# Performance work log

Hardware: AMD Instinct MI355X
Metric: run time of the kernel (lower is better)

The kernel has to match this reference:

```python
import jax, jax.numpy as jnp
import numpy as np


def _pool2(x):
    # 2x2 max pool, stride 2 (matches F.max_pool2d(x, 2))
    b, c, h, w = x.shape
    return x.reshape(b, c, h // 2, 2, w // 2, 2).max(axis=(3, 5))


def setup_inputs() -> dict:
    key = jax.random.key(0)
    ks = jax.random.split(key, 6)
    B, C, H, W = 16, 512, 64, 64
    x = jax.random.normal(ks[0], (B, C, H, W), dtype=jnp.float32)
    scale = 0.02
    theta_w = jax.random.normal(ks[1], (C // 8, C), dtype=jnp.float32) * scale
    phi_w = jax.random.normal(ks[2], (C // 8, C), dtype=jnp.float32) * scale
    g_w = jax.random.normal(ks[3], (C // 2, C), dtype=jnp.float32) * scale
    o_w = jax.random.normal(ks[4], (C, C // 2), dtype=jnp.float32) * scale
    # original inits gamma=0; use a nonzero value so output depends on attention path
    gamma = jax.random.normal(ks[5], (), dtype=jnp.float32) * 0.5
    return {"x": x, "theta_w": theta_w, "phi_w": phi_w, "g_w": g_w, "o_w": o_w, "gamma": gamma}


def reference(x, theta_w, phi_w, g_w, o_w, gamma):
    B, C, H, W = x.shape
    HW = H * W
    # 1x1 convs == channel GEMMs
    theta = jnp.einsum('bchw,kc->bkhw', x, theta_w).reshape(B, C // 8, HW).transpose(0, 2, 1)  # [B, HW, C/8]
    phi = _pool2(jnp.einsum('bchw,kc->bkhw', x, phi_w)).reshape(B, C // 8, HW // 4)            # [B, C/8, HW/4]
    beta = jax.nn.softmax(jnp.einsum('bnk,bkm->bnm', theta, phi), axis=-1)                     # [B, HW, HW/4]
    g = _pool2(jnp.einsum('bchw,kc->bkhw', x, g_w)).reshape(B, C // 2, HW // 4)                # [B, C/2, HW/4]
    # g.bmm(beta^T): contract over pooled positions m -> [B, C/2, HW]
    o_in = jnp.einsum('bcm,bnm->bcn', g, beta).reshape(B, C // 2, H, W)
    o = jnp.einsum('bchw,kc->bkhw', o_in, o_w)                                                 # [B, C, H, W]
    return gamma * o + x
```

## Files before the change

### kernel.cpp

```cpp
#include <hip/hip_runtime.h>

#define B_   16
#define C_   512
#define HW_  4096
#define M_   1024
#define TPAD 136

typedef __attribute__((ext_vector_type(8))) short bf16x8;
typedef __attribute__((ext_vector_type(4))) float f32x4;

static __device__ __forceinline__ unsigned short f2bf(float f) {
    union { float f; unsigned u; } v; v.f = f;
    unsigned r = v.u + 0x7fffu + ((v.u >> 16) & 1u);
    return (unsigned short)(r >> 16);
}
static __device__ __forceinline__ float bf2f(unsigned short h) {
    union { unsigned u; float f; } v; v.u = ((unsigned)h) << 16;
    return v.f;
}
static __device__ __forceinline__ void gload_lds16(const void* g, void* l) {
    __builtin_amdgcn_global_load_lds(
        (const __attribute__((address_space(1))) unsigned int*)g,
        (__attribute__((address_space(3))) unsigned int*)l, 16, 0, 0);
}

__global__ __launch_bounds__(256) void k_weights(
    const float* __restrict__ thw, const float* __restrict__ phw,
    const float* __restrict__ gw,  const float* __restrict__ ow,
    unsigned short* __restrict__ Wb, unsigned short* __restrict__ oWb,
    unsigned short* __restrict__ g_p) {
    int i = blockIdx.x * 256 + threadIdx.x;
    if (i < 32768)        Wb[i] = f2bf(thw[i]);
    else if (i < 65536)   Wb[i] = f2bf(phw[i - 32768]);
    else if (i < 196608)  Wb[i] = f2bf(gw[i - 65536]);
    else if (i < 327680)  oWb[i - 196608] = f2bf(ow[i - 196608]);
    else if (i < 589824) {
        int i2 = i - 327680;
        int b = i2 >> 14;
        int r = (i2 >> 10) & 15;
        int m = i2 & 1023;
        g_p[((size_t)b * 272 + 256 + r) * M_ + m] =
            (r == 0) ? (unsigned short)0x3F80u : (unsigned short)0;
    }
}

__global__ __launch_bounds__(256) void k_transpose_x(
    const float* __restrict__ x, unsigned short* __restrict__ xT) {
    __shared__ float tile[64][65];
    int b = blockIdx.z, c0 = blockIdx.y * 64, hw0 = blockIdx.x * 64;
    const float* xb = x + ((size_t)b * C_ + c0) * HW_ + hw0;
    int t = threadIdx.x;
    int r = t >> 4, c4 = (t & 15) * 4;
#pragma unroll
    for (int k = 0; k < 4; k++) {
        int row = r + k * 16;
        float4 v = *reinterpret_cast<const float4*>(xb + (size_t)row * HW_ + c4);
        tile[row][c4 + 0] = v.x; tile[row][c4 + 1] = v.y;
        tile[row][c4 + 2] = v.z; tile[row][c4 + 3] = v.w;
    }
    __syncthreads();
    unsigned short* o = xT + ((size_t)b * HW_ + hw0) * C_ + c0;
#pragma unroll
    for (int k = 0; k < 4; k++) {
        int hwr = r + k * 16;
        ushort4 u;
        u.x = f2bf(tile[c4 + 0][hwr]); u.y = f2bf(tile[c4 + 1][hwr]);
        u.z = f2bf(tile[c4 + 2][hwr]); u.w = f2bf(tile[c4 + 3][hwr]);
        *reinterpret_cast<ushort4*>(o + (size_t)hwr * C_ + c4) = u;
    }
}

__global__ __launch_bounds__(256, 4) void k_proj(
    const unsigned short* __restrict__ xT, const unsigned short* __restrict__ Wb,
    unsigned short* __restrict__ theta_n, unsigned short* __restrict__ phi_p,
    unsigned short* __restrict__ g_p) {
    __shared__ unsigned short smem[128 * TPAD];
    unsigned short* As = smem;
    unsigned short* Bs = smem + 8192;

    int b = blockIdx.z, mt = blockIdx.y, bx = blockIdx.x;
    int hw0 = bx * 128;
    int tid = threadIdx.x, w = tid >> 6, lane = tid & 63;
    int l15 = lane & 15, q = lane >> 4;
    int wr = w >> 1, wc = w & 1;

    const unsigned short* Ab = Wb + (size_t)(mt * 128) * 512;
    const unsigned short* Bb = xT + ((size_t)b * HW_ + hw0) * 512;
    int trow = tid >> 3, tch = tid & 7;

    f32x4 acc[4][4] = {};
    for (int ks = 0; ks < 8; ks++) {
        int k0 = ks * 64;
        if (ks) __syncthreads();
#pragma unroll
        for (int i = 0; i < 4; i++) {
            int row = i * 32 + trow;
            int ch = tch ^ (row & 7);
            gload_lds16(Ab + (size_t)row * 512 + k0 + ch * 8, &As[(i * 256 + w * 64) * 8]);
        }
#pragma unroll
        for (int i = 0; i < 4; i++) {
            int row = i * 32 + trow;
            int ch = tch ^ (row & 7);
            gload_lds16(Bb + (size_t)row * 512 + k0 + ch * 8, &Bs[(i * 256 + w * 64) * 8]);
        }
        __syncthreads();
#pragma unroll
        for (int kk = 0; kk < 2; kk++) {
            bf16x8 af[4], bfr[4];
#pragma unroll
            for (int mi = 0; mi < 4; mi++) {
                int row = wr * 64 + mi * 16 + l15;
                int ch = (kk * 4 + q) ^ (row & 7);
                af[mi] = *(const bf16x8*)&As[row * 64 + ch * 8];
            }
#pragma unroll
            for (int ni = 0; ni < 4; ni++) {
                int row = wc * 64 + ni * 16 + l15;
                int ch = (kk * 4 + q) ^ (row & 7);
                bfr[ni] = *(const bf16x8*)&Bs[row * 64 + ch * 8];
            }
#pragma unroll
            for (int mi = 0; mi < 4; mi++)
#pragma unroll
                for (int ni = 0; ni < 4; ni++)
                    acc[mi][ni] = __builtin_amdgcn_mfma_f32_16x16x32_bf16(
                        af[mi], bfr[ni], acc[mi][ni], 0, 0, 0);
        }
    }

    __syncthreads();
#pragma unroll
    for (int mi = 0; mi < 4; mi++)
#pragma unroll
        for (int ni = 0; ni < 4; ni++) {
            int col = wc * 64 + ni * 16 + l15;
            int row = wr * 64 + mi * 16 + q * 4;
            ushort4 u;
            u.x = f2bf(acc[mi][ni][0]); u.y = f2bf(acc[mi][ni][1]);
            u.z = f2bf(acc[mi][ni][2]); u.w = f2bf(acc[mi][ni][3]);
            *reinterpret_cast<ushort4*>(&smem[col * TPAD + row]) = u;
        }
    __syncthreads();

    if (mt == 0) {
        int hw_l = tid >> 1, kh = (tid & 1) * 32;
        const unsigned short* srcp = &smem[hw_l * TPAD + kh];
        unsigned short* dstp = theta_n + ((size_t)b * HW_ + hw0 + hw_l) * 64 + kh;
#pragma unroll
        for (int i = 0; i < 4; i++)
            *reinterpret_cast<uint4*>(dstp + i * 8) =
                *reinterpret_cast<const uint4*>(srcp + i * 8);
        int pc = tid & 63, mg = tid >> 6;
#pragma unroll
        for (int j = 0; j < 8; j++) {
            int m_l = mg * 8 + j, w_ = m_l * 2;
            float v0 = bf2f(smem[(w_)      * TPAD + 64 + pc]);
            float v1 = bf2f(smem[(w_ + 1)  * TPAD + 64 + pc]);
            float v2 = bf2f(smem[(64 + w_) * TPAD + 64 + pc]);
            float v3 = bf2f(smem[(65 + w_) * TPAD + 64 + pc]);
            float v = fmaxf(fmaxf(v0, v1), fmaxf(v2, v3));
            phi_p[((size_t)b * M_ + bx * 32 + m_l) * 64 + pc] = f2bf(v);
        }
    } else {
        int lr = tid & 127, half = tid >> 7;
        int gc = (mt - 1) * 128 + lr;
        unsigned short* dst = g_p + ((size_t)b * 272 + gc) * M_ + bx * 32 + half * 16;
        unsigned short tmp[16];
#pragma unroll
        for (int i = 0; i < 16; i++) {
            int w_ = (half * 16 + i) * 2;
            float v0 = bf2f(smem[(w_)      * TPAD + lr]);
            float v1 = bf2f(smem[(w_ + 1)  * TPAD + lr]);
            float v2 = bf2f(smem[(64 + w_) * TPAD + lr]);
            float v3 = bf2f(smem[(65 + w_) * TPAD + lr]);
            tmp[i] = f2bf(fmaxf(fmaxf(v0, v1), fmaxf(v2, v3)));
        }
#pragma unroll
        for (int i = 0; i < 4; i++)
            *reinterpret_cast<ushort4*>(dst + i * 4) =
                *reinterpret_cast<const ushort4*>(&tmp[i * 4]);
    }
}

__global__ __launch_bounds__(512, 4) void k_attn(
    const unsigned short* __restrict__ theta_n, const unsigned short* __restrict__ phi_p,
    const unsigned short* __restrict__ g_p, unsigned short* __restrict__ o_in) {
    __shared__ unsigned short phi_s[64 * 64];
    __shared__ unsigned short g_s[272 * 64];
    __shared__ unsigned short p_lds[8][16][88];

    int b = blockIdx.y, n0 = blockIdx.x * 128;
    int tid = threadIdx.x, w = tid >> 6, lane = tid & 63;
    int l15 = lane & 15, q = lane >> 4;
    int nw = n0 + w * 16;

    const unsigned short* th = theta_n + ((size_t)b * HW_ + nw + l15) * 64 + q * 8;
    bf16x8 a0 = *(const bf16x8*)(th);
    bf16x8 a1 = *(const bf16x8*)(th + 32);

    const unsigned short* phib = phi_p + (size_t)b * M_ * 64;
    const unsigned short* gb   = g_p   + (size_t)b * 272 * M_;

    int sw = l15 & 7;

    f32x4 acc[17] = {};
    for (int mc = 0; mc < 16; mc++) {
        int m0 = mc * 64;
        __syncthreads();
        {
            int p = tid;
            int row = p >> 3, ch = (p & 7) ^ (row & 7);
            gload_lds16(phib + (size_t)(m0 + row) * 64 + ch * 8, &phi_s[w * 512]);
        }
#pragma unroll
        for (int it = 0; it < 5; it++) {
            int s = w + it * 8;
            if (s < 34) {
                int row = s * 8 + (lane >> 3);
                int ch = (lane & 7) ^ (row & 7);
                gload_lds16(gb + (size_t)row * M_ + m0 + ch * 8, &g_s[s * 512]);
            }
        }
        __syncthreads();

#pragma unroll
        for (int f = 0; f < 4; f++) {
            const unsigned short* pr = &phi_s[(f * 16 + l15) * 64];
            bf16x8 b0 = *(const bf16x8*)(pr + (q ^ sw) * 8);
            bf16x8 b1 = *(const bf16x8*)(pr + ((q + 4) ^ sw) * 8);
            f32x4 s = {};
            s = __builtin_amdgcn_mfma_f32_16x16x32_bf16(a0, b0, s, 0, 0, 0);
            s = __builtin_amdgcn_mfma_f32_16x16x32_bf16(a1, b1, s, 0, 0, 0);
#pragma unroll
            for (int j = 0; j < 4; j++)
                p_lds[w][q * 4 + j][f * 16 + l15] = f2bf(__expf(s[j]));
        }
        bf16x8 p0 = *(const bf16x8*)&p_lds[w][l15][q * 8];
        bf16x8 p1 = *(const bf16x8*)&p_lds[w][l15][32 + q * 8];
#pragma unroll
        for (int cf = 0; cf < 17; cf++) {
            const unsigned short* gr = &g_s[(cf * 16 + l15) * 64];
            bf16x8 g0 = *(const bf16x8*)(gr + (q ^ sw) * 8);
            bf16x8 g1 = *(const bf16x8*)(gr + ((q + 4) ^ sw) * 8);
            acc[cf] = __builtin_amdgcn_mfma_f32_16x16x32_bf16(p0, g0, acc[cf], 0, 0, 0);
            acc[cf] = __builtin_amdgcn_mfma_f32_16x16x32_bf16(p1, g1, acc[cf], 0, 0, 0);
        }
    }

    float dinv[4];
#pragma unroll
    for (int j = 0; j < 4; j++) {
        float d = __shfl(acc[16][j], (lane & 48), 64);
        dinv[j] = 1.0f / d;
    }
#pragma unroll
    for (int cf = 0; cf < 16; cf++)
#pragma unroll
        for (int j = 0; j < 4; j++)
            o_in[((size_t)b * HW_ + nw + q * 4 + j) * 256 + cf * 16 + l15] =
                f2bf(acc[cf][j] * dinv[j]);
}

__global__ __launch_bounds__(256, 4) void k_oproj(
    const unsigned short* __restrict__ o_in, const unsigned short* __restrict__ oWb,
    const float* __restrict__ x, const float* __restrict__ gamma_p,
    float* __restrict__ out) {
    __shared__ unsigned short smem[128 * TPAD];
    unsigned short* As = smem;
    unsigned short* Bs = smem + 8192;

    int b = blockIdx.z, mt = blockIdx.y, hw0 = blockIdx.x * 128;
    int tid = threadIdx.x, w = tid >> 6, lane = tid & 63;
    int l15 = lane & 15, q = lane >> 4;
    int wr = w >> 1, wc = w & 1;

    const unsigned short* Ab = oWb + (size_t)(mt * 128) * 256;
    const unsigned short* Bb = o_in + ((size_t)b * HW_ + hw0) * 256;
    int trow = tid >> 3, tch = tid & 7;

    f32x4 acc[4][4] = {};
    for (int ks = 0; ks < 4; ks++) {
        int k0 = ks * 64;
        if (ks) __syncthreads();
#pragma unroll
        for (int i = 0; i < 4; i++) {
            int row = i * 32 + trow;
            int ch = tch ^ (row & 7);
            gload_lds16(Ab + (size_t)row * 256 + k0 + ch * 8, &As[(i * 256 + w * 64) * 8]);
        }
#pragma unroll
        for (int i = 0; i < 4; i++) {
            int row = i * 32 + trow;
            int ch = tch ^ (row & 7);
            gload_lds16(Bb + (size_t)row * 256 + k0 + ch * 8, &Bs[(i * 256 + w * 64) * 8]);
        }
        __syncthreads();
#pragma unroll
        for (int kk = 0; kk < 2; kk++) {
            bf16x8 af[4], bfr[4];
#pragma unroll
            for (int mi = 0; mi < 4; mi++) {
                int row = wr * 64 + mi * 16 + l15;
                int ch = (kk * 4 + q) ^ (row & 7);
                af[mi] = *(const bf16x8*)&As[row * 64 + ch * 8];
            }
#pragma unroll
            for (int ni = 0; ni < 4; ni++) {
                int row = wc * 64 + ni * 16 + l15;
                int ch = (kk * 4 + q) ^ (row & 7);
                bfr[ni] = *(const bf16x8*)&Bs[row * 64 + ch * 8];
            }
#pragma unroll
            for (int mi = 0; mi < 4; mi++)
#pragma unroll
                for (int ni = 0; ni < 4; ni++)
                    acc[mi][ni] = __builtin_amdgcn_mfma_f32_16x16x32_bf16(
                        af[mi], bfr[ni], acc[mi][ni], 0, 0, 0);
        }
    }

    __syncthreads();
#pragma unroll
    for (int mi = 0; mi < 4; mi++)
#pragma unroll
        for (int ni = 0; ni < 4; ni++) {
            int col = wc * 64 + ni * 16 + l15;
            int rb = wr * 64 + mi * 16 + q * 4;
#pragma unroll
            for (int j = 0; j < 4; j++)
                smem[(rb + j) * TPAD + col] = f2bf(acc[mi][ni][j]);
        }
    __syncthreads();

    float gam = *gamma_p;
    int sub = tid >> 5, p32 = tid & 31;
#pragma unroll
    for (int p = 0; p < 16; p++) {
        int row = p * 8 + sub;
        ushort4 v = *reinterpret_cast<const ushort4*>(&smem[row * TPAD + p32 * 4]);
        size_t idx = ((size_t)b * C_ + mt * 128 + row) * HW_ + hw0 + p32 * 4;
        float4 xv = *reinterpret_cast<const float4*>(x + idx);
        float4 o;
        o.x = gam * bf2f(v.x) + xv.x;
        o.y = gam * bf2f(v.y) + xv.y;
        o.z = gam * bf2f(v.z) + xv.z;
        o.w = gam * bf2f(v.w) + xv.w;
        *reinterpret_cast<float4*>(out + idx) = o;
    }
}

extern "C" void kernel_launch(void* const* d_in, const int* in_sizes, int n_in,
                              void* d_out, int out_size, void* d_ws, size_t ws_size,
                              hipStream_t stream) {
    const float* x     = (const float*)d_in[0];
    const float* thw   = (const float*)d_in[1];
    const float* phw   = (const float*)d_in[2];
    const float* gw    = (const float*)d_in[3];
    const float* ow    = (const float*)d_in[4];
    const float* gamma = (const float*)d_in[5];
    float* out = (float*)d_out;

    char* ws = (char*)d_ws;
    unsigned short* xT   = (unsigned short*)(ws + 0);
    unsigned short* Wb   = (unsigned short*)(ws + 67108864);
    unsigned short* oWb  = (unsigned short*)(ws + 67502080);
    unsigned short* oin  = (unsigned short*)(ws + 67764224);
    unsigned short* thn  = (unsigned short*)(ws + 118095872);
    unsigned short* phip = (unsigned short*)(ws + 126484480);
    unsigned short* gp   = (unsigned short*)(ws + 128581632);

    hipLaunchKernelGGL(k_weights, dim3(2304), dim3(256), 0, stream, thw, phw, gw, ow, Wb, oWb, gp);
    hipLaunchKernelGGL(k_transpose_x, dim3(64, 8, 16), dim3(256), 0, stream, x, xT);
    hipLaunchKernelGGL(k_proj, dim3(32, 3, 16), dim3(256), 0, stream, xT, Wb, thn, phip, gp);
    hipLaunchKernelGGL(k_attn, dim3(32, 16), dim3(512), 0, stream, thn, phip, gp, oin);
    hipLaunchKernelGGL(k_oproj, dim3(32, 4, 16), dim3(256), 0, stream, oin, oWb, x, gamma, out);
}
```

Measured before the change: 193.6 us.

## Fuse x transpose and bf16 conversion into projection GEMM tile loads

Removes the separate transpose kernel and the bf16 xT workspace. The projection GEMM now reads fp32 x directly, converts it to bf16 and transposes it into swizzled LDS with a new bank-swizzle function. This avoids the intermediate round trip to global memory and one launch. In exchange it reads fp32 x for each of the three weight tiles and replaces async global-to-LDS loads with synchronous register loads and LDS stores.

```diff
diff --git a/kernel.cpp b/kernel.cpp
--- a/kernel.cpp
+++ b/kernel.cpp
@@ -23,6 +23,7 @@
         (const __attribute__((address_space(1))) unsigned int*)g,
         (__attribute__((address_space(3))) unsigned int*)l, 16, 0, 0);
 }
+static __device__ __forceinline__ int fb(int row) { return (row ^ (row >> 2)) & 7; }
 
 __global__ __launch_bounds__(256) void k_weights(
     const float* __restrict__ thw, const float* __restrict__ phw,
@@ -44,34 +45,8 @@
     }
 }
 
-__global__ __launch_bounds__(256) void k_transpose_x(
-    const float* __restrict__ x, unsigned short* __restrict__ xT) {
-    __shared__ float tile[64][65];
-    int b = blockIdx.z, c0 = blockIdx.y * 64, hw0 = blockIdx.x * 64;
-    const float* xb = x + ((size_t)b * C_ + c0) * HW_ + hw0;
-    int t = threadIdx.x;
-    int r = t >> 4, c4 = (t & 15) * 4;
-#pragma unroll
-    for (int k = 0; k < 4; k++) {
-        int row = r + k * 16;
-        float4 v = *reinterpret_cast<const float4*>(xb + (size_t)row * HW_ + c4);
-        tile[row][c4 + 0] = v.x; tile[row][c4 + 1] = v.y;
-        tile[row][c4 + 2] = v.z; tile[row][c4 + 3] = v.w;
-    }
-    __syncthreads();
-    unsigned short* o = xT + ((size_t)b * HW_ + hw0) * C_ + c0;
-#pragma unroll
-    for (int k = 0; k < 4; k++) {
-        int hwr = r + k * 16;
-        ushort4 u;
-        u.x = f2bf(tile[c4 + 0][hwr]); u.y = f2bf(tile[c4 + 1][hwr]);
-        u.z = f2bf(tile[c4 + 2][hwr]); u.w = f2bf(tile[c4 + 3][hwr]);
-        *reinterpret_cast<ushort4*>(o + (size_t)hwr * C_ + c4) = u;
-    }
-}
-
 __global__ __launch_bounds__(256, 4) void k_proj(
-    const unsigned short* __restrict__ xT, const unsigned short* __restrict__ Wb,
+    const float* __restrict__ x, const unsigned short* __restrict__ Wb,
     unsigned short* __restrict__ theta_n, unsigned short* __restrict__ phi_p,
     unsigned short* __restrict__ g_p) {
     __shared__ unsigned short smem[128 * TPAD];
@@ -85,8 +60,10 @@
     int wr = w >> 1, wc = w & 1;
 
     const unsigned short* Ab = Wb + (size_t)(mt * 128) * 512;
-    const unsigned short* Bb = xT + ((size_t)b * HW_ + hw0) * 512;
+    const float* xb = x + (size_t)b * C_ * HW_ + hw0;
     int trow = tid >> 3, tch = tid & 7;
+    int hg4 = (tid & 31) * 4;
+    int kq2 = (tid >> 5) * 2;
 
     f32x4 acc[4][4] = {};
     for (int ks = 0; ks < 8; ks++) {
@@ -99,10 +76,24 @@
             gload_lds16(Ab + (size_t)row * 512 + k0 + ch * 8, &As[(i * 256 + w * 64) * 8]);
         }
 #pragma unroll
-        for (int i = 0; i < 4; i++) {
-            int row = i * 32 + trow;
-            int ch = tch ^ (row & 7);
-            gload_lds16(Bb + (size_t)row * 512 + k0 + ch * 8, &Bs[(i * 256 + w * 64) * 8]);
+        for (int it = 0; it < 2; it++) {
+            int kg = kq2 + it;
+            const float* xs = xb + (size_t)(k0 + kg * 4) * HW_ + hg4;
+            float4 r0 = *reinterpret_cast<const float4*>(xs);
+            float4 r1 = *reinterpret_cast<const float4*>(xs + HW_);
+            float4 r2 = *reinterpret_cast<const float4*>(xs + 2 * HW_);
+            float4 r3 = *reinterpret_cast<const float4*>(xs + 3 * HW_);
+            const float* p0 = (const float*)&r0; const float* p1 = (const float*)&r1;
+            const float* p2 = (const float*)&r2; const float* p3 = (const float*)&r3;
+#pragma unroll
+            for (int t = 0; t < 4; t++) {
+                int row = hg4 + t;
+                int ch = (kg >> 1) ^ fb(row);
+                ushort4 u;
+                u.x = f2bf(p0[t]); u.y = f2bf(p1[t]);
+                u.z = f2bf(p2[t]); u.w = f2bf(p3[t]);
+                *reinterpret_cast<ushort4*>(&Bs[row * 64 + ch * 8 + (kg & 1) * 4]) = u;
+            }
         }
         __syncthreads();
 #pragma unroll
@@ -117,7 +108,7 @@
 #pragma unroll
             for (int ni = 0; ni < 4; ni++) {
                 int row = wc * 64 + ni * 16 + l15;
-                int ch = (kk * 4 + q) ^ (row & 7);
+                int ch = (kk * 4 + q) ^ fb(row);
                 bfr[ni] = *(const bf16x8*)&Bs[row * 64 + ch * 8];
             }
 #pragma unroll
@@ -362,17 +353,15 @@
     float* out = (float*)d_out;
 
     char* ws = (char*)d_ws;
-    unsigned short* xT   = (unsigned short*)(ws + 0);
-    unsigned short* Wb   = (unsigned short*)(ws + 67108864);
-    unsigned short* oWb  = (unsigned short*)(ws + 67502080);
-    unsigned short* oin  = (unsigned short*)(ws + 67764224);
-    unsigned short* thn  = (unsigned short*)(ws + 118095872);
-    unsigned short* phip = (unsigned short*)(ws + 126484480);
-    unsigned short* gp   = (unsigned short*)(ws + 128581632);
+    unsigned short* Wb   = (unsigned short*)(ws + 0);
+    unsigned short* oWb  = (unsigned short*)(ws + 393216);
+    unsigned short* oin  = (unsigned short*)(ws + 655360);
+    unsigned short* thn  = (unsigned short*)(ws + 34209792);
+    unsigned short* phip = (unsigned short*)(ws + 42598400);
+    unsigned short* gp   = (unsigned short*)(ws + 44695552);
 
     hipLaunchKernelGGL(k_weights, dim3(2304), dim3(256), 0, stream, thw, phw, gw, ow, Wb, oWb, gp);
-    hipLaunchKernelGGL(k_transpose_x, dim3(64, 8, 16), dim3(256), 0, stream, x, xT);
-    hipLaunchKernelGGL(k_proj, dim3(32, 3, 16), dim3(256), 0, stream, xT, Wb, thn, phip, gp);
+    hipLaunchKernelGGL(k_proj, dim3(32, 3, 16), dim3(256), 0, stream, x, Wb, thn, phip, gp);
     hipLaunchKernelGGL(k_attn, dim3(32, 16), dim3(512), 0, stream, thn, phip, gp, oin);
     hipLaunchKernelGGL(k_oproj, dim3(32, 4, 16), dim3(256), 0, stream, oin, oWb, x, gamma, out);
 }
```

Result: slower. 198.9 us (+2.7%).

## Double-buffer attention tiles and compute softmax denominator from register ones

Applied to the files above, without the earlier changes.

The attention kernel now streams phi and g in 32-wide chunks into two LDS buffers, prefetching the next chunk while computing the current one, with one barrier per iteration. The softmax row-sum, previously obtained from padded ones-rows in g_p written by the weight kernel, is now computed by an extra MFMA against an in-register ones vector. The padding-row initialization and its threads are dropped. This aims to hide global-to-LDS load latency and cut LDS traffic, at the cost of twice as many loop iterations with smaller MFMA batches. Workspace offsets are also moved.

```diff
diff --git a/kernel.cpp b/kernel.cpp
--- a/kernel.cpp
+++ b/kernel.cpp
@@ -27,21 +27,12 @@
 __global__ __launch_bounds__(256) void k_weights(
     const float* __restrict__ thw, const float* __restrict__ phw,
     const float* __restrict__ gw,  const float* __restrict__ ow,
-    unsigned short* __restrict__ Wb, unsigned short* __restrict__ oWb,
-    unsigned short* __restrict__ g_p) {
+    unsigned short* __restrict__ Wb, unsigned short* __restrict__ oWb) {
     int i = blockIdx.x * 256 + threadIdx.x;
     if (i < 32768)        Wb[i] = f2bf(thw[i]);
     else if (i < 65536)   Wb[i] = f2bf(phw[i - 32768]);
     else if (i < 196608)  Wb[i] = f2bf(gw[i - 65536]);
     else if (i < 327680)  oWb[i - 196608] = f2bf(ow[i - 196608]);
-    else if (i < 589824) {
-        int i2 = i - 327680;
-        int b = i2 >> 14;
-        int r = (i2 >> 10) & 15;
-        int m = i2 & 1023;
-        g_p[((size_t)b * 272 + 256 + r) * M_ + m] =
-            (r == 0) ? (unsigned short)0x3F80u : (unsigned short)0;
-    }
 }
 
 __global__ __launch_bounds__(256) void k_transpose_x(
@@ -186,9 +177,9 @@
 __global__ __launch_bounds__(512, 4) void k_attn(
     const unsigned short* __restrict__ theta_n, const unsigned short* __restrict__ phi_p,
     const unsigned short* __restrict__ g_p, unsigned short* __restrict__ o_in) {
-    __shared__ unsigned short phi_s[64 * 64];
-    __shared__ unsigned short g_s[272 * 64];
-    __shared__ unsigned short p_lds[8][16][88];
+    __shared__ unsigned short g_s[2][256 * 32];
+    __shared__ unsigned short phi_s[2][32 * 64];
+    __shared__ unsigned short p_lds[8][16][40];
 
     int b = blockIdx.y, n0 = blockIdx.x * 128;
     int tid = threadIdx.x, w = tid >> 6, lane = tid & 63;
@@ -202,31 +193,41 @@
     const unsigned short* phib = phi_p + (size_t)b * M_ * 64;
     const unsigned short* gb   = g_p   + (size_t)b * 272 * M_;
 
+    bf16x8 ones;
+    {
+        short v = (l15 == 0) ? (short)0x3F80 : (short)0;
+#pragma unroll
+        for (int i = 0; i < 8; i++) ones[i] = v;
+    }
+
+#define STAGE(mc_, bufi_)                                                      \
+    {                                                                          \
+        int m0_ = (mc_) * 32;                                                  \
+        _Pragma("unroll")                                                      \
+        for (int i = 0; i < 2; i++) {                                          \
+            int u = w * 128 + i * 64 + lane;                                   \
+            int row = u >> 2, ch = (u & 3) ^ (row & 3);                        \
+            gload_lds16(gb + (size_t)row * M_ + m0_ + ch * 8,                  \
+                        &g_s[bufi_][(w * 128 + i * 64) * 8]);                  \
+        }                                                                      \
+        if (w < 4) {                                                           \
+            int u = w * 64 + lane;                                             \
+            int row = u >> 3, ch = (u & 7) ^ (row & 7);                        \
+            gload_lds16(phib + (size_t)(m0_ + row) * 64 + ch * 8,              \
+                        &phi_s[bufi_][w * 512]);                               \
+        }                                                                      \
+    }
+
+    f32x4 acc[17] = {};
+    STAGE(0, 0);
+    __syncthreads();
     int sw = l15 & 7;
-
-    f32x4 acc[17] = {};
-    for (int mc = 0; mc < 16; mc++) {
-        int m0 = mc * 64;
-        __syncthreads();
-        {
-            int p = tid;
-            int row = p >> 3, ch = (p & 7) ^ (row & 7);
-            gload_lds16(phib + (size_t)(m0 + row) * 64 + ch * 8, &phi_s[w * 512]);
-        }
-#pragma unroll
-        for (int it = 0; it < 5; it++) {
-            int s = w + it * 8;
-            if (s < 34) {
-                int row = s * 8 + (lane >> 3);
-                int ch = (lane & 7) ^ (row & 7);
-                gload_lds16(gb + (size_t)row * M_ + m0 + ch * 8, &g_s[s * 512]);
-            }
-        }
-        __syncthreads();
-
-#pragma unroll
-        for (int f = 0; f < 4; f++) {
-            const unsigned short* pr = &phi_s[(f * 16 + l15) * 64];
+    for (int mc = 0; mc < 32; mc++) {
+        int cur = mc & 1;
+        if (mc < 31) STAGE(mc + 1, cur ^ 1);
+#pragma unroll
+        for (int f = 0; f < 2; f++) {
+            const unsigned short* pr = &phi_s[cur][(f * 16 + l15) * 64];
             bf16x8 b0 = *(const bf16x8*)(pr + (q ^ sw) * 8);
             bf16x8 b1 = *(const bf16x8*)(pr + ((q + 4) ^ sw) * 8);
             f32x4 s = {};
@@ -237,16 +238,16 @@
                 p_lds[w][q * 4 + j][f * 16 + l15] = f2bf(__expf(s[j]));
         }
         bf16x8 p0 = *(const bf16x8*)&p_lds[w][l15][q * 8];
-        bf16x8 p1 = *(const bf16x8*)&p_lds[w][l15][32 + q * 8];
-#pragma unroll
-        for (int cf = 0; cf < 17; cf++) {
-            const unsigned short* gr = &g_s[(cf * 16 + l15) * 64];
-            bf16x8 g0 = *(const bf16x8*)(gr + (q ^ sw) * 8);
-            bf16x8 g1 = *(const bf16x8*)(gr + ((q + 4) ^ sw) * 8);
+#pragma unroll
+        for (int cf = 0; cf < 16; cf++) {
+            int grow = cf * 16 + l15;
+            bf16x8 g0 = *(const bf16x8*)&g_s[cur][grow * 32 + ((q ^ (grow & 3)) * 8)];
             acc[cf] = __builtin_amdgcn_mfma_f32_16x16x32_bf16(p0, g0, acc[cf], 0, 0, 0);
-            acc[cf] = __builtin_amdgcn_mfma_f32_16x16x32_bf16(p1, g1, acc[cf], 0, 0, 0);
-        }
-    }
+        }
+        acc[16] = __builtin_amdgcn_mfma_f32_16x16x32_bf16(p0, ones, acc[16], 0, 0, 0);
+        __syncthreads();
+    }
+#undef STAGE
 
     float dinv[4];
 #pragma unroll
@@ -366,11 +367,11 @@
     unsigned short* Wb   = (unsigned short*)(ws + 67108864);
     unsigned short* oWb  = (unsigned short*)(ws + 67502080);
     unsigned short* oin  = (unsigned short*)(ws + 67764224);
-    unsigned short* thn  = (unsigned short*)(ws + 118095872);
-    unsigned short* phip = (unsigned short*)(ws + 126484480);
-    unsigned short* gp   = (unsigned short*)(ws + 128581632);
-
-    hipLaunchKernelGGL(k_weights, dim3(2304), dim3(256), 0, stream, thw, phw, gw, ow, Wb, oWb, gp);
+    unsigned short* thn  = (unsigned short*)(ws + 101318656);
+    unsigned short* phip = (unsigned short*)(ws + 109707264);
+    unsigned short* gp   = (unsigned short*)(ws + 111804416);
+
+    hipLaunchKernelGGL(k_weights, dim3(1280), dim3(256), 0, stream, thw, phw, gw, ow, Wb, oWb);
     hipLaunchKernelGGL(k_transpose_x, dim3(64, 8, 16), dim3(256), 0, stream, x, xT);
     hipLaunchKernelGGL(k_proj, dim3(32, 3, 16), dim3(256), 0, stream, xT, Wb, thn, phip, gp);
     hipLaunchKernelGGL(k_attn, dim3(32, 16), dim3(512), 0, stream, thn, phip, gp, oin);
```

Result: slower. 200.7 us (+3.7%).

## Give each attention wave two query tiles and synthesize the ones column in registers

Applied to the files above, without the earlier changes.

The attention kernel now runs 4 waves of 256 threads per block, each handling 32 query rows as two 16-row tiles. Every g/phi fragment read from LDS is reused by both tiles, which halves LDS fragment traffic per MFMA. The extra ones/zero rows appended to g_p for the softmax denominator are dropped: a register 'ones' operand feeds the denominator MFMA instead, so k_weights no longer writes them and the g buffer shrinks to 256 rows. The cost is twice the accumulator registers per wave and fewer waves per block, which may lower occupancy and latency hiding.

```diff
diff --git a/kernel.cpp b/kernel.cpp
--- a/kernel.cpp
+++ b/kernel.cpp
@@ -27,21 +27,12 @@
 __global__ __launch_bounds__(256) void k_weights(
     const float* __restrict__ thw, const float* __restrict__ phw,
     const float* __restrict__ gw,  const float* __restrict__ ow,
-    unsigned short* __restrict__ Wb, unsigned short* __restrict__ oWb,
-    unsigned short* __restrict__ g_p) {
+    unsigned short* __restrict__ Wb, unsigned short* __restrict__ oWb) {
     int i = blockIdx.x * 256 + threadIdx.x;
     if (i < 32768)        Wb[i] = f2bf(thw[i]);
     else if (i < 65536)   Wb[i] = f2bf(phw[i - 32768]);
     else if (i < 196608)  Wb[i] = f2bf(gw[i - 65536]);
     else if (i < 327680)  oWb[i - 196608] = f2bf(ow[i - 196608]);
-    else if (i < 589824) {
-        int i2 = i - 327680;
-        int b = i2 >> 14;
-        int r = (i2 >> 10) & 15;
-        int m = i2 & 1023;
-        g_p[((size_t)b * 272 + 256 + r) * M_ + m] =
-            (r == 0) ? (unsigned short)0x3F80u : (unsigned short)0;
-    }
 }
 
 __global__ __launch_bounds__(256) void k_transpose_x(
@@ -165,7 +156,7 @@
     } else {
         int lr = tid & 127, half = tid >> 7;
         int gc = (mt - 1) * 128 + lr;
-        unsigned short* dst = g_p + ((size_t)b * 272 + gc) * M_ + bx * 32 + half * 16;
+        unsigned short* dst = g_p + ((size_t)b * 256 + gc) * M_ + bx * 32 + half * 16;
         unsigned short tmp[16];
 #pragma unroll
         for (int i = 0; i < 16; i++) {
@@ -183,44 +174,52 @@
     }
 }
 
-__global__ __launch_bounds__(512, 4) void k_attn(
+__global__ __launch_bounds__(256, 2) void k_attn(
     const unsigned short* __restrict__ theta_n, const unsigned short* __restrict__ phi_p,
     const unsigned short* __restrict__ g_p, unsigned short* __restrict__ o_in) {
     __shared__ unsigned short phi_s[64 * 64];
-    __shared__ unsigned short g_s[272 * 64];
-    __shared__ unsigned short p_lds[8][16][88];
+    __shared__ unsigned short g_s[256 * 64];
+    __shared__ unsigned short p_lds[4][32][68];
 
     int b = blockIdx.y, n0 = blockIdx.x * 128;
     int tid = threadIdx.x, w = tid >> 6, lane = tid & 63;
     int l15 = lane & 15, q = lane >> 4;
-    int nw = n0 + w * 16;
+    int nw = n0 + w * 32;
 
     const unsigned short* th = theta_n + ((size_t)b * HW_ + nw + l15) * 64 + q * 8;
-    bf16x8 a0 = *(const bf16x8*)(th);
-    bf16x8 a1 = *(const bf16x8*)(th + 32);
+    bf16x8 a[2][2];
+    a[0][0] = *(const bf16x8*)(th);            a[0][1] = *(const bf16x8*)(th + 32);
+    a[1][0] = *(const bf16x8*)(th + 16 * 64);  a[1][1] = *(const bf16x8*)(th + 16 * 64 + 32);
 
     const unsigned short* phib = phi_p + (size_t)b * M_ * 64;
-    const unsigned short* gb   = g_p   + (size_t)b * 272 * M_;
+    const unsigned short* gb   = g_p   + (size_t)b * 256 * M_;
+
+    bf16x8 ones;
+    {
+        short v = (l15 == 0) ? (short)0x3F80 : (short)0;
+#pragma unroll
+        for (int i = 0; i < 8; i++) ones[i] = v;
+    }
 
     int sw = l15 & 7;
 
-    f32x4 acc[17] = {};
+    f32x4 acc[2][17] = {};
     for (int mc = 0; mc < 16; mc++) {
         int m0 = mc * 64;
         __syncthreads();
-        {
-            int p = tid;
-            int row = p >> 3, ch = (p & 7) ^ (row & 7);
-            gload_lds16(phib + (size_t)(m0 + row) * 64 + ch * 8, &phi_s[w * 512]);
-        }
-#pragma unroll
-        for (int it = 0; it < 5; it++) {
-            int s = w + it * 8;
-            if (s < 34) {
-                int row = s * 8 + (lane >> 3);
-                int ch = (lane & 7) ^ (row & 7);
-                gload_lds16(gb + (size_t)row * M_ + m0 + ch * 8, &g_s[s * 512]);
-            }
+#pragma unroll
+        for (int i = 0; i < 2; i++) {
+            int u = i * 256 + tid;
+            int row = u >> 3, ch = (lane & 7) ^ (row & 7);
+            gload_lds16(phib + (size_t)(m0 + row) * 64 + ch * 8,
+                        &phi_s[(i * 256 + w * 64) * 8]);
+        }
+#pragma unroll
+        for (int i = 0; i < 8; i++) {
+            int u = i * 256 + tid;
+            int row = u >> 3, ch = (lane & 7) ^ (row & 7);
+            gload_lds16(gb + (size_t)row * M_ + m0 + ch * 8,
+                        &g_s[(i * 256 + w * 64) * 8]);
         }
         __syncthreads();
 
@@ -229,37 +228,55 @@
             const unsigned short* pr = &phi_s[(f * 16 + l15) * 64];
             bf16x8 b0 = *(const bf16x8*)(pr + (q ^ sw) * 8);
             bf16x8 b1 = *(const bf16x8*)(pr + ((q + 4) ^ sw) * 8);
-            f32x4 s = {};
-            s = __builtin_amdgcn_mfma_f32_16x16x32_bf16(a0, b0, s, 0, 0, 0);
-            s = __builtin_amdgcn_mfma_f32_16x16x32_bf16(a1, b1, s, 0, 0, 0);
-#pragma unroll
-            for (int j = 0; j < 4; j++)
-                p_lds[w][q * 4 + j][f * 16 + l15] = f2bf(__expf(s[j]));
-        }
-        bf16x8 p0 = *(const bf16x8*)&p_lds[w][l15][q * 8];
-        bf16x8 p1 = *(const bf16x8*)&p_lds[w][l15][32 + q * 8];
-#pragma unroll
-        for (int cf = 0; cf < 17; cf++) {
+#pragma unroll
+            for (int t = 0; t < 2; t++) {
+                f32x4 s = {};
+                s = __builtin_amdgcn_mfma_f32_16x16x32_bf16(a[t][0], b0, s, 0, 0, 0);
+                s = __builtin_amdgcn_mfma_f32_16x16x32_bf16(a[t][1], b1, s, 0, 0, 0);
+#pragma unroll
+                for (int j = 0; j < 4; j++)
+                    p_lds[w][t * 16 + q * 4 + j][f * 16 + l15] = f2bf(__expf(s[j]));
+            }
+        }
+        bf16x8 p[2][2];
+#pragma unroll
+        for (int t = 0; t < 2; t++) {
+            p[t][0] = *(const bf16x8*)&p_lds[w][t * 16 + l15][q * 8];
+            p[t][1] = *(const bf16x8*)&p_lds[w][t * 16 + l15][32 + q * 8];
+        }
+#pragma unroll
+        for (int cf = 0; cf < 16; cf++) {
             const unsigned short* gr = &g_s[(cf * 16 + l15) * 64];
             bf16x8 g0 = *(const bf16x8*)(gr + (q ^ sw) * 8);
             bf16x8 g1 = *(const bf16x8*)(gr + ((q + 4) ^ sw) * 8);
-            acc[cf] = __builtin_amdgcn_mfma_f32_16x16x32_bf16(p0, g0, acc[cf], 0, 0, 0);
-            acc[cf] = __builtin_amdgcn_mfma_f32_16x16x32_bf16(p1, g1, acc[cf], 0, 0, 0);
-        }
-    }
-
-    float dinv[4];
-#pragma unroll
-    for (int j = 0; j < 4; j++) {
-        float d = __shfl(acc[16][j], (lane & 48), 64);
-        dinv[j] = 1.0f / d;
-    }
-#pragma unroll
-    for (int cf = 0; cf < 16; cf++)
-#pragma unroll
-        for (int j = 0; j < 4; j++)
-            o_in[((size_t)b * HW_ + nw + q * 4 + j) * 256 + cf * 16 + l15] =
-                f2bf(acc[cf][j] * dinv[j]);
+#pragma unroll
+            for (int t = 0; t < 2; t++) {
+                acc[t][cf] = __builtin_amdgcn_mfma_f32_16x16x32_bf16(p[t][0], g0, acc[t][cf], 0, 0, 0);
+                acc[t][cf] = __builtin_amdgcn_mfma_f32_16x16x32_bf16(p[t][1], g1, acc[t][cf], 0, 0, 0);
+            }
+        }
+#pragma unroll
+        for (int t = 0; t < 2; t++) {
+            acc[t][16] = __builtin_amdgcn_mfma_f32_16x16x32_bf16(p[t][0], ones, acc[t][16], 0, 0, 0);
+            acc[t][16] = __builtin_amdgcn_mfma_f32_16x16x32_bf16(p[t][1], ones, acc[t][16], 0, 0, 0);
+        }
+    }
+
+#pragma unroll
+    for (int t = 0; t < 2; t++) {
+        float dinv[4];
+#pragma unroll
+        for (int j = 0; j < 4; j++) {
+            float d = __shfl(acc[t][16][j], (lane & 48), 64);
+            dinv[j] = 1.0f / d;
+        }
+#pragma unroll
+        for (int cf = 0; cf < 16; cf++)
+#pragma unroll
+            for (int j = 0; j < 4; j++)
+                o_in[((size_t)b * HW_ + nw + t * 16 + q * 4 + j) * 256 + cf * 16 + l15] =
+                    f2bf(acc[t][cf][j] * dinv[j]);
+    }
 }
 
 __global__ __launch_bounds__(256, 4) void k_oproj(
@@ -366,13 +383,13 @@
     unsigned short* Wb   = (unsigned short*)(ws + 67108864);
     unsigned short* oWb  = (unsigned short*)(ws + 67502080);
     unsigned short* oin  = (unsigned short*)(ws + 67764224);
-    unsigned short* thn  = (unsigned short*)(ws + 118095872);
-    unsigned short* phip = (unsigned short*)(ws + 126484480);
-    unsigned short* gp   = (unsigned short*)(ws + 128581632);
-
-    hipLaunchKernelGGL(k_weights, dim3(2304), dim3(256), 0, stream, thw, phw, gw, ow, Wb, oWb, gp);
+    unsigned short* thn  = (unsigned short*)(ws + 101318656);
+    unsigned short* phip = (unsigned short*)(ws + 109707264);
+    unsigned short* gp   = (unsigned short*)(ws + 111804416);
+
+    hipLaunchKernelGGL(k_weights, dim3(1280), dim3(256), 0, stream, thw, phw, gw, ow, Wb, oWb);
     hipLaunchKernelGGL(k_transpose_x, dim3(64, 8, 16), dim3(256), 0, stream, x, xT);
     hipLaunchKernelGGL(k_proj, dim3(32, 3, 16), dim3(256), 0, stream, xT, Wb, thn, phip, gp);
-    hipLaunchKernelGGL(k_attn, dim3(32, 16), dim3(512), 0, stream, thn, phip, gp, oin);
+    hipLaunchKernelGGL(k_attn, dim3(32, 16), dim3(256), 0, stream, thn, phip, gp, oin);
     hipLaunchKernelGGL(k_oproj, dim3(32, 4, 16), dim3(256), 0, stream, oin, oWb, x, gamma, out);
 }
```

After: 192.3 us. Within noise of the previous version (-0.7%).
